# Performance work log

Hardware: AMD Instinct MI355X
Metric: run time of the kernel (lower is better)

## Reference

```python
import jax, jax.numpy as jnp
import numpy as np

EMBEDDING_DIM = 100
M = 50                      # chunk width
NUM_CHUNK = EMBEDDING_DIM // M  # 2
VOCAB = 100000
EPS = 1e-8                  # torch CosineSimilarity eps


def setup_inputs() -> dict:
    key = jax.random.key(0)
    k_idx, k_emb, k_w, k_u = jax.random.split(key, 4)
    word_idxs = jax.random.randint(k_idx, (4096, 200), 0, VOCAB)  # [B, L]
    # embedding table initialized uniform(-1, 1) as in the original np.random.uniform
    emb_table = jax.random.uniform(k_emb, (VOCAB, EMBEDDING_DIM), dtype=jnp.float32,
                                   minval=-1.0, maxval=1.0)
    weights = jnp.ones((EMBEDDING_DIM, 1), dtype=jnp.float32)      # output projection
    attend_u = jnp.ones((NUM_CHUNK, M), dtype=jnp.float32)         # per-chunk attention query
    return {"word_idxs": word_idxs, "emb_table": emb_table,
            "weights": weights, "attend_u": attend_u}


def reference(word_idxs, emb_table, weights, attend_u):
    B, L = word_idxs.shape
    embeds = emb_table[word_idxs]                       # [B, L, 100]
    ch = embeds.reshape(B, L, NUM_CHUNK, M)             # [B, L, C, M]
    # cosine similarity per word vs per-chunk query (torch eps semantics)
    e_norm = ch / jnp.maximum(jnp.linalg.norm(ch, axis=-1, keepdims=True), EPS)
    u_norm = attend_u / jnp.maximum(jnp.linalg.norm(attend_u, axis=-1, keepdims=True), EPS)
    cos = jnp.einsum('blcm,cm->blc', e_norm, u_norm)    # [B, L, C]
    alphas = jnp.exp(cos)                               # positive -> L1 norm == sum
    norm_alphas = alphas / jnp.sum(alphas, axis=1, keepdims=True)
    hidden = jnp.einsum('blcm,blc->bcm', ch, norm_alphas).reshape(B, EMBEDDING_DIM)
    return hidden @ weights                             # [B, 1]
```

## Files before the change

### kernel.cpp

```cpp
#include <hip/hip_runtime.h>

constexpr int C_ = 2;
constexpr int M_ = 50;
constexpr int ED = 100;
constexpr float EPS = 1e-8f;


__global__ __launch_bounds__(256) void row_stats_kernel(
    const float* __restrict__ emb,
    const float* __restrict__ wgt,
    const float* __restrict__ att,
    float*       __restrict__ tbl,
    int vocab)
{
    __shared__ float2 s_uw[ED];
    __shared__ float  s_su[C_];

    const int t = threadIdx.x;
    if (t < ED) s_uw[t] = make_float2(att[t], wgt[t]);
    __syncthreads();
    if (t < C_) {
        float ss = 0.f;
        #pragma unroll
        for (int m = 0; m < M_; ++m) { float v = s_uw[t * M_ + m].x; ss += v * v; }
        s_su[t] = 1.0f / fmaxf(sqrtf(ss), EPS);
    }
    __syncthreads();

    const int r = blockIdx.x * 256 + t;
    if (r >= vocab) return;

    const float4* rowp = reinterpret_cast<const float4*>(emb + (long long)r * ED);

    float sq0 = 0.f, du0 = 0.f, dw0 = 0.f;
    float sq1 = 0.f, du1 = 0.f, dw1 = 0.f;

    #pragma unroll
    for (int j = 0; j < 25; ++j) {
        const float4 v = rowp[j];
        const float vals[4] = { v.x, v.y, v.z, v.w };
        #pragma unroll
        for (int k = 0; k < 4; ++k) {
            const int e = 4 * j + k;
            const float2 uw = s_uw[e];
            const float x = vals[k];
            if (e < M_) {
                sq0 = fmaf(x, x, sq0);
                du0 = fmaf(x, uw.x, du0);
                dw0 = fmaf(x, uw.y, dw0);
            } else {
                sq1 = fmaf(x, x, sq1);
                du1 = fmaf(x, uw.x, du1);
                dw1 = fmaf(x, uw.y, dw1);
            }
        }
    }

    const float cos0 = du0 / fmaxf(sqrtf(sq0), EPS) * s_su[0];
    const float cos1 = du1 / fmaxf(sqrtf(sq1), EPS) * s_su[1];
    const float a0 = __expf(cos0);
    const float a1 = __expf(cos1);

    reinterpret_cast<float4*>(tbl)[r] = make_float4(a0, a0 * dw0, a1, a1 * dw1);
}

__global__ __launch_bounds__(256) void attend_kernel(
    const int*    __restrict__ idx,
    const float4* __restrict__ tbl,
    float*        __restrict__ out,
    int B, int L)
{
    const int wave = threadIdx.x >> 6;
    const int lane = threadIdx.x & 63;
    const int b    = blockIdx.x * 4 + wave;
    if (b >= B) return;

    const int* ib = idx + (long long)b * L;
    float a0 = 0.f, a1 = 0.f, ap0 = 0.f, ap1 = 0.f;
    #pragma unroll 4
    for (int l = lane; l < L; l += 64) {
        const float4 v = tbl[ib[l]];
        a0 += v.x; ap0 += v.y; a1 += v.z; ap1 += v.w;
    }

    #pragma unroll
    for (int off = 32; off > 0; off >>= 1) {
        a0  += __shfl_down(a0,  off, 64);
        a1  += __shfl_down(a1,  off, 64);
        ap0 += __shfl_down(ap0, off, 64);
        ap1 += __shfl_down(ap1, off, 64);
    }
    if (lane == 0) out[b] = ap0 / a0 + ap1 / a1;
}

extern "C" void kernel_launch(void* const* d_in, const int* in_sizes, int n_in,
                              void* d_out, int out_size, void* d_ws, size_t ws_size,
                              hipStream_t stream) {
    const int*   idx = (const int*)d_in[0];
    const float* emb = (const float*)d_in[1];
    const float* wgt = (const float*)d_in[2];
    const float* att = (const float*)d_in[3];
    float* out = (float*)d_out;

    const int B     = out_size;
    const int L     = in_sizes[0] / B;
    const int vocab = in_sizes[1] / ED;

    float* tbl = (float*)d_ws;

    row_stats_kernel<<<(vocab + 255) / 256, 256, 0, stream>>>(emb, wgt, att, tbl, vocab);
    attend_kernel<<<(B + 3) / 4, 256, 0, stream>>>(idx, (const float4*)tbl, out, B, L);
}
```

Baseline: 96.00 us.

## Split each embedding row across four lanes and use two waves per batch row

The row-stats kernel now gives each vocab row to four adjacent lanes. Each lane reads interleaved float4s and the partial sums are combined with xor shuffles, so global loads are more coalesced than the previous one-thread-per-row 400-byte strided reads. The attend kernel now spreads each batch row over two waves and combines them through shared memory, which gives more memory parallelism per row. In exchange it adds shuffle reductions, idle lanes during the tail and final writes, and a block-level sync.

Measured after the change: 92.54 us. 3.6% less time.

```diff
diff --git a/kernel.cpp b/kernel.cpp
--- a/kernel.cpp
+++ b/kernel.cpp
@@ -27,7 +27,11 @@
     }
     __syncthreads();
 
-    const int r = blockIdx.x * 256 + t;
+    const int wave = t >> 6;
+    const int lane = t & 63;
+    const int g    = lane >> 2;
+    const int j    = lane & 3;
+    const int r    = blockIdx.x * 64 + wave * 16 + g;
     if (r >= vocab) return;
 
     const float4* rowp = reinterpret_cast<const float4*>(emb + (long long)r * ED);
@@ -36,32 +40,51 @@
     float sq1 = 0.f, du1 = 0.f, dw1 = 0.f;
 
     #pragma unroll
-    for (int j = 0; j < 25; ++j) {
-        const float4 v = rowp[j];
-        const float vals[4] = { v.x, v.y, v.z, v.w };
+    for (int it = 0; it < 6; ++it) {
+        const float4 v = rowp[4 * it + j];
+        const float xs[4] = { v.x, v.y, v.z, v.w };
         #pragma unroll
         for (int k = 0; k < 4; ++k) {
-            const int e = 4 * j + k;
-            const float2 uw = s_uw[e];
-            const float x = vals[k];
-            if (e < M_) {
-                sq0 = fmaf(x, x, sq0);
-                du0 = fmaf(x, uw.x, du0);
-                dw0 = fmaf(x, uw.y, dw0);
+            const int ebase = 16 * it + k;
+            const float x   = xs[k];
+            const float2 uw = s_uw[ebase + 4 * j];
+            if (ebase + 12 < M_) {
+                sq0 = fmaf(x, x, sq0); du0 = fmaf(x, uw.x, du0); dw0 = fmaf(x, uw.y, dw0);
+            } else if (ebase >= M_) {
+                sq1 = fmaf(x, x, sq1); du1 = fmaf(x, uw.x, du1); dw1 = fmaf(x, uw.y, dw1);
             } else {
-                sq1 = fmaf(x, x, sq1);
-                du1 = fmaf(x, uw.x, du1);
-                dw1 = fmaf(x, uw.y, dw1);
+                if (j == 0) { sq0 = fmaf(x, x, sq0); du0 = fmaf(x, uw.x, du0); dw0 = fmaf(x, uw.y, dw0); }
+                else        { sq1 = fmaf(x, x, sq1); du1 = fmaf(x, uw.x, du1); dw1 = fmaf(x, uw.y, dw1); }
             }
         }
     }
+    if (j == 0) {
+        const float4 v = rowp[24];
+        const float xs[4] = { v.x, v.y, v.z, v.w };
+        #pragma unroll
+        for (int k = 0; k < 4; ++k) {
+            const float2 uw = s_uw[96 + k];
+            sq1 = fmaf(xs[k], xs[k], sq1); du1 = fmaf(xs[k], uw.x, du1); dw1 = fmaf(xs[k], uw.y, dw1);
+        }
+    }
 
-    const float cos0 = du0 / fmaxf(sqrtf(sq0), EPS) * s_su[0];
-    const float cos1 = du1 / fmaxf(sqrtf(sq1), EPS) * s_su[1];
-    const float a0 = __expf(cos0);
-    const float a1 = __expf(cos1);
+    #pragma unroll
+    for (int m = 1; m < 4; m <<= 1) {
+        sq0 += __shfl_xor(sq0, m, 4);
+        du0 += __shfl_xor(du0, m, 4);
+        dw0 += __shfl_xor(dw0, m, 4);
+        sq1 += __shfl_xor(sq1, m, 4);
+        du1 += __shfl_xor(du1, m, 4);
+        dw1 += __shfl_xor(dw1, m, 4);
+    }
 
-    reinterpret_cast<float4*>(tbl)[r] = make_float4(a0, a0 * dw0, a1, a1 * dw1);
+    if (j == 0) {
+        const float cos0 = du0 / fmaxf(sqrtf(sq0), EPS) * s_su[0];
+        const float cos1 = du1 / fmaxf(sqrtf(sq1), EPS) * s_su[1];
+        const float a0 = __expf(cos0);
+        const float a1 = __expf(cos1);
+        reinterpret_cast<float4*>(tbl)[r] = make_float4(a0, a0 * dw0, a1, a1 * dw1);
+    }
 }
 
 __global__ __launch_bounds__(256) void attend_kernel(
@@ -70,27 +93,38 @@
     float*        __restrict__ out,
     int B, int L)
 {
-    const int wave = threadIdx.x >> 6;
-    const int lane = threadIdx.x & 63;
-    const int b    = blockIdx.x * 4 + wave;
-    if (b >= B) return;
+    __shared__ float4 s_part[4];
 
-    const int* ib = idx + (long long)b * L;
-    float a0 = 0.f, a1 = 0.f, ap0 = 0.f, ap1 = 0.f;
-    #pragma unroll 4
-    for (int l = lane; l < L; l += 64) {
-        const float4 v = tbl[ib[l]];
-        a0 += v.x; ap0 += v.y; a1 += v.z; ap1 += v.w;
+    const int half = threadIdx.x >> 7;
+    const int tt   = threadIdx.x & 127;
+    const int b    = blockIdx.x * 2 + half;
+
+    float a0 = 0.f, ap0 = 0.f, a1 = 0.f, ap1 = 0.f;
+    if (b < B) {
+        const int* ib = idx + (long long)b * L;
+        #pragma unroll 2
+        for (int l = tt; l < L; l += 128) {
+            const float4 v = tbl[ib[l]];
+            a0 += v.x; ap0 += v.y; a1 += v.z; ap1 += v.w;
+        }
+        #pragma unroll
+        for (int off = 32; off > 0; off >>= 1) {
+            a0  += __shfl_down(a0,  off, 64);
+            a1  += __shfl_down(a1,  off, 64);
+            ap0 += __shfl_down(ap0, off, 64);
+            ap1 += __shfl_down(ap1, off, 64);
+        }
     }
 
-    #pragma unroll
-    for (int off = 32; off > 0; off >>= 1) {
-        a0  += __shfl_down(a0,  off, 64);
-        a1  += __shfl_down(a1,  off, 64);
-        ap0 += __shfl_down(ap0, off, 64);
-        ap1 += __shfl_down(ap1, off, 64);
+    const int wave = threadIdx.x >> 6;
+    if ((threadIdx.x & 63) == 0) s_part[wave] = make_float4(a0, ap0, a1, ap1);
+    __syncthreads();
+
+    if (tt == 0 && b < B) {
+        const float4 p = s_part[half * 2];
+        const float4 q = s_part[half * 2 + 1];
+        out[b] = (p.y + q.y) / (p.x + q.x) + (p.w + q.w) / (p.z + q.z);
     }
-    if (lane == 0) out[b] = ap0 / a0 + ap1 / a1;
 }
 
 extern "C" void kernel_launch(void* const* d_in, const int* in_sizes, int n_in,
@@ -108,6 +142,6 @@
 
     float* tbl = (float*)d_ws;
 
-    row_stats_kernel<<<(vocab + 255) / 256, 256, 0, stream>>>(emb, wgt, att, tbl, vocab);
-    attend_kernel<<<(B + 3) / 4, 256, 0, stream>>>(idx, (const float4*)tbl, out, B, L);
+    row_stats_kernel<<<(vocab + 63) / 64, 256, 0, stream>>>(emb, wgt, att, tbl, vocab);
+    attend_kernel<<<(B + 1) / 2, 256, 0, stream>>>(idx, (const float4*)tbl, out, B, L);
 }
```

## Split each vocab row across four lanes for coalesced row-stats loads

Applied to the files above, without the earlier changes.

The row-stats kernel now gives each vocab row to a group of four adjacent lanes, each handling two rows, instead of one whole row per thread. Neighbouring lanes read neighbouring float4s, so the 40MB embedding table is read with far better coalescing than the old strided per-thread 400-byte row walks. Partial sums are combined with 4-lane xor shuffles, and the chunk boundary that falls inside a float4 is handled by lane index. The cost is more shuffle work, extra registers, and some lane divergence on the tail float4.

New measurement: 93.06 us. 3.1% less time.

```diff
diff --git a/kernel.cpp b/kernel.cpp
--- a/kernel.cpp
+++ b/kernel.cpp
@@ -27,41 +27,97 @@
     }
     __syncthreads();
 
-    const int r = blockIdx.x * 256 + t;
-    if (r >= vocab) return;
+    const int wave = t >> 6;
+    const int lane = t & 63;
+    const int g    = lane >> 2;
+    const int j    = lane & 3;
+    const int rA   = blockIdx.x * 128 + wave * 32 + g;
+    const int rB   = rA + 16;
+    const bool okA = (rA < vocab);
+    const bool okB = (rB < vocab);
+    if (!okA) return;
 
-    const float4* rowp = reinterpret_cast<const float4*>(emb + (long long)r * ED);
+    const float4* rpA = reinterpret_cast<const float4*>(emb + (long long)rA * ED);
+    const float4* rpB = reinterpret_cast<const float4*>(emb + (long long)rB * ED);
 
-    float sq0 = 0.f, du0 = 0.f, dw0 = 0.f;
-    float sq1 = 0.f, du1 = 0.f, dw1 = 0.f;
+    float4 va[6], vb[6];
+    #pragma unroll
+    for (int it = 0; it < 6; ++it) va[it] = rpA[4 * it + j];
+    if (okB) {
+        #pragma unroll
+        for (int it = 0; it < 6; ++it) vb[it] = rpB[4 * it + j];
+    }
+    float4 ta, tb;
+    if (j == 0) {
+        ta = rpA[24];
+        if (okB) tb = rpB[24];
+    }
+
+    float AsQ0 = 0.f, AdU0 = 0.f, AdW0 = 0.f, AsQ1 = 0.f, AdU1 = 0.f, AdW1 = 0.f;
+    float BsQ0 = 0.f, BdU0 = 0.f, BdW0 = 0.f, BsQ1 = 0.f, BdU1 = 0.f, BdW1 = 0.f;
 
     #pragma unroll
-    for (int j = 0; j < 25; ++j) {
-        const float4 v = rowp[j];
-        const float vals[4] = { v.x, v.y, v.z, v.w };
+    for (int it = 0; it < 6; ++it) {
+        const float xsA[4] = { va[it].x, va[it].y, va[it].z, va[it].w };
+        const float xsB[4] = { vb[it].x, vb[it].y, vb[it].z, vb[it].w };
         #pragma unroll
         for (int k = 0; k < 4; ++k) {
-            const int e = 4 * j + k;
-            const float2 uw = s_uw[e];
-            const float x = vals[k];
-            if (e < M_) {
-                sq0 = fmaf(x, x, sq0);
-                du0 = fmaf(x, uw.x, du0);
-                dw0 = fmaf(x, uw.y, dw0);
+            const int ebase = 16 * it + k;
+            const float2 uw = s_uw[ebase + 4 * j];
+            const float xA = xsA[k];
+            const float xB = xsB[k];
+            if (ebase + 12 < M_) {
+                AsQ0 = fmaf(xA, xA, AsQ0); AdU0 = fmaf(xA, uw.x, AdU0); AdW0 = fmaf(xA, uw.y, AdW0);
+                BsQ0 = fmaf(xB, xB, BsQ0); BdU0 = fmaf(xB, uw.x, BdU0); BdW0 = fmaf(xB, uw.y, BdW0);
+            } else if (ebase >= M_) {
+                AsQ1 = fmaf(xA, xA, AsQ1); AdU1 = fmaf(xA, uw.x, AdU1); AdW1 = fmaf(xA, uw.y, AdW1);
+                BsQ1 = fmaf(xB, xB, BsQ1); BdU1 = fmaf(xB, uw.x, BdU1); BdW1 = fmaf(xB, uw.y, BdW1);
             } else {
-                sq1 = fmaf(x, x, sq1);
-                du1 = fmaf(x, uw.x, du1);
-                dw1 = fmaf(x, uw.y, dw1);
+                if (j == 0) {
+                    AsQ0 = fmaf(xA, xA, AsQ0); AdU0 = fmaf(xA, uw.x, AdU0); AdW0 = fmaf(xA, uw.y, AdW0);
+                    BsQ0 = fmaf(xB, xB, BsQ0); BdU0 = fmaf(xB, uw.x, BdU0); BdW0 = fmaf(xB, uw.y, BdW0);
+                } else {
+                    AsQ1 = fmaf(xA, xA, AsQ1); AdU1 = fmaf(xA, uw.x, AdU1); AdW1 = fmaf(xA, uw.y, AdW1);
+                    BsQ1 = fmaf(xB, xB, BsQ1); BdU1 = fmaf(xB, uw.x, BdU1); BdW1 = fmaf(xB, uw.y, BdW1);
+                }
             }
         }
     }
+    if (j == 0) {
+        const float xsA[4] = { ta.x, ta.y, ta.z, ta.w };
+        const float xsB[4] = { tb.x, tb.y, tb.z, tb.w };
+        #pragma unroll
+        for (int k = 0; k < 4; ++k) {
+            const float2 uw = s_uw[96 + k];
+            AsQ1 = fmaf(xsA[k], xsA[k], AsQ1); AdU1 = fmaf(xsA[k], uw.x, AdU1); AdW1 = fmaf(xsA[k], uw.y, AdW1);
+            BsQ1 = fmaf(xsB[k], xsB[k], BsQ1); BdU1 = fmaf(xsB[k], uw.x, BdU1); BdW1 = fmaf(xsB[k], uw.y, BdW1);
+        }
+    }
 
-    const float cos0 = du0 / fmaxf(sqrtf(sq0), EPS) * s_su[0];
-    const float cos1 = du1 / fmaxf(sqrtf(sq1), EPS) * s_su[1];
-    const float a0 = __expf(cos0);
-    const float a1 = __expf(cos1);
+    #pragma unroll
+    for (int m = 1; m < 4; m <<= 1) {
+        AsQ0 += __shfl_xor(AsQ0, m, 4); AdU0 += __shfl_xor(AdU0, m, 4); AdW0 += __shfl_xor(AdW0, m, 4);
+        AsQ1 += __shfl_xor(AsQ1, m, 4); AdU1 += __shfl_xor(AdU1, m, 4); AdW1 += __shfl_xor(AdW1, m, 4);
+        BsQ0 += __shfl_xor(BsQ0, m, 4); BdU0 += __shfl_xor(BdU0, m, 4); BdW0 += __shfl_xor(BdW0, m, 4);
+        BsQ1 += __shfl_xor(BsQ1, m, 4); BdU1 += __shfl_xor(BdU1, m, 4); BdW1 += __shfl_xor(BdW1, m, 4);
+    }
 
-    reinterpret_cast<float4*>(tbl)[r] = make_float4(a0, a0 * dw0, a1, a1 * dw1);
+    if (j == 0) {
+        {
+            const float cos0 = AdU0 / fmaxf(sqrtf(AsQ0), EPS) * s_su[0];
+            const float cos1 = AdU1 / fmaxf(sqrtf(AsQ1), EPS) * s_su[1];
+            const float a0 = __expf(cos0);
+            const float a1 = __expf(cos1);
+            reinterpret_cast<float4*>(tbl)[rA] = make_float4(a0, a0 * AdW0, a1, a1 * AdW1);
+        }
+        if (okB) {
+            const float cos0 = BdU0 / fmaxf(sqrtf(BsQ0), EPS) * s_su[0];
+            const float cos1 = BdU1 / fmaxf(sqrtf(BsQ1), EPS) * s_su[1];
+            const float a0 = __expf(cos0);
+            const float a1 = __expf(cos1);
+            reinterpret_cast<float4*>(tbl)[rB] = make_float4(a0, a0 * BdW0, a1, a1 * BdW1);
+        }
+    }
 }
 
 __global__ __launch_bounds__(256) void attend_kernel(
@@ -108,6 +164,6 @@
 
     float* tbl = (float*)d_ws;
 
-    row_stats_kernel<<<(vocab + 255) / 256, 256, 0, stream>>>(emb, wgt, att, tbl, vocab);
+    row_stats_kernel<<<(vocab + 127) / 128, 256, 0, stream>>>(emb, wgt, att, tbl, vocab);
     attend_kernel<<<(B + 3) / 4, 256, 0, stream>>>(idx, (const float4*)tbl, out, B, L);
 }
```

## Fuse row statistics and attention into one per-batch gather kernel

Applied to the files above, without the earlier changes.

Drops the per-vocabulary precomputation kernel and its workspace table. Each wave now handles one batch row: groups of four lanes gather a full 100-float embedding row, compute the chunk norms and dot products with shuffle reductions, and accumulate the exp-weighted sums directly. This removes a kernel launch and the pass over the whole table. In exchange it reads a full 400-byte row for every token instead of a 16-byte precomputed entry, and repeats the per-row maths for every occurrence of a word.

Measured after the change: 130.8 us. 1.36x slower.

```diff
diff --git a/kernel.cpp b/kernel.cpp
--- a/kernel.cpp
+++ b/kernel.cpp
@@ -5,92 +5,120 @@
 constexpr int ED = 100;
 constexpr float EPS = 1e-8f;
 
-
-__global__ __launch_bounds__(256) void row_stats_kernel(
+__global__ __launch_bounds__(256) void fused_direct_kernel(
+    const int*   __restrict__ idx,
     const float* __restrict__ emb,
     const float* __restrict__ wgt,
     const float* __restrict__ att,
-    float*       __restrict__ tbl,
-    int vocab)
+    float*       __restrict__ out,
+    int B, int L)
 {
-    __shared__ float2 s_uw[ED];
-    __shared__ float  s_su[C_];
+    __shared__ float s_su[C_];
 
     const int t = threadIdx.x;
-    if (t < ED) s_uw[t] = make_float2(att[t], wgt[t]);
-    __syncthreads();
     if (t < C_) {
         float ss = 0.f;
         #pragma unroll
-        for (int m = 0; m < M_; ++m) { float v = s_uw[t * M_ + m].x; ss += v * v; }
+        for (int m = 0; m < M_; ++m) { const float v = att[t * M_ + m]; ss += v * v; }
         s_su[t] = 1.0f / fmaxf(sqrtf(ss), EPS);
     }
     __syncthreads();
 
-    const int r = blockIdx.x * 256 + t;
-    if (r >= vocab) return;
+    const int wv   = t >> 6;
+    const int lane = t & 63;
+    const int g    = lane >> 2;
+    const int j    = lane & 3;
+    const int b    = blockIdx.x * 4 + wv;
+    if (b >= B) return;
 
-    const float4* rowp = reinterpret_cast<const float4*>(emb + (long long)r * ED);
+    const float su0 = s_su[0], su1 = s_su[1];
 
-    float sq0 = 0.f, du0 = 0.f, dw0 = 0.f;
-    float sq1 = 0.f, du1 = 0.f, dw1 = 0.f;
+    const float4* att4 = reinterpret_cast<const float4*>(att);
+    const float4* wgt4 = reinterpret_cast<const float4*>(wgt);
+    float4 uf[7], wf[7];
+    #pragma unroll
+    for (int k = 0; k < 7; ++k) {
+        const int f = j + 4 * k;
+        if (f < 25) { uf[k] = att4[f]; wf[k] = wgt4[f]; }
+        else        { uf[k] = make_float4(0.f,0.f,0.f,0.f); wf[k] = uf[k]; }
+    }
 
-    #pragma unroll
-    for (int j = 0; j < 25; ++j) {
-        const float4 v = rowp[j];
-        const float vals[4] = { v.x, v.y, v.z, v.w };
+    const int*    ib   = idx + (long long)b * L;
+    const float4* emb4 = reinterpret_cast<const float4*>(emb);
+
+    float A0 = 0.f, AP0 = 0.f, A1 = 0.f, AP1 = 0.f;
+
+    for (int base = 0; base < L; base += 256) {
+        int pre[4];
         #pragma unroll
-        for (int k = 0; k < 4; ++k) {
-            const int e = 4 * j + k;
-            const float2 uw = s_uw[e];
-            const float x = vals[k];
-            if (e < M_) {
-                sq0 = fmaf(x, x, sq0);
-                du0 = fmaf(x, uw.x, du0);
-                dw0 = fmaf(x, uw.y, dw0);
-            } else {
-                sq1 = fmaf(x, x, sq1);
-                du1 = fmaf(x, uw.x, du1);
-                dw1 = fmaf(x, uw.y, dw1);
+        for (int m = 0; m < 4; ++m) {
+            const int l0 = base + 64 * m + lane;
+            pre[m] = (l0 < L) ? ib[l0] : 0;
+        }
+        #pragma unroll
+        for (int i = 0; i < 16; ++i) {
+            if (base + 16 * i >= L) break;
+            const int ridx = __shfl(pre[i >> 2], 16 * (i & 3) + g, 64);
+            const int l    = base + 16 * i + g;
+            if (l < L) {
+                const float4* rp = emb4 + (long long)ridx * 25;
+                float4 rv[7];
+                #pragma unroll
+                for (int k = 0; k < 6; ++k) rv[k] = rp[j + 4 * k];
+                if (j == 0) rv[6] = rp[24];
+
+                float sq0 = 0.f, du0 = 0.f, dw0 = 0.f;
+                float sq1 = 0.f, du1 = 0.f, dw1 = 0.f;
+                #pragma unroll
+                for (int k = 0; k < 6; ++k) {
+                    const float xs[4] = { rv[k].x, rv[k].y, rv[k].z, rv[k].w };
+                    const float us[4] = { uf[k].x, uf[k].y, uf[k].z, uf[k].w };
+                    const float ws[4] = { wf[k].x, wf[k].y, wf[k].z, wf[k].w };
+                    #pragma unroll
+                    for (int c = 0; c < 4; ++c) {
+                        const float x = xs[c];
+                        if (k <= 2) {
+                            sq0 = fmaf(x, x, sq0); du0 = fmaf(x, us[c], du0); dw0 = fmaf(x, ws[c], dw0);
+                        } else if (k >= 4) {
+                            sq1 = fmaf(x, x, sq1); du1 = fmaf(x, us[c], du1); dw1 = fmaf(x, ws[c], dw1);
+                        } else {
+                            if (j == 0 && c < 2) { sq0 = fmaf(x, x, sq0); du0 = fmaf(x, us[c], du0); dw0 = fmaf(x, ws[c], dw0); }
+                            else                 { sq1 = fmaf(x, x, sq1); du1 = fmaf(x, us[c], du1); dw1 = fmaf(x, ws[c], dw1); }
+                        }
+                    }
+                }
+                if (j == 0) {
+                    const float xs[4] = { rv[6].x, rv[6].y, rv[6].z, rv[6].w };
+                    const float us[4] = { uf[6].x, uf[6].y, uf[6].z, uf[6].w };
+                    const float ws[4] = { wf[6].x, wf[6].y, wf[6].z, wf[6].w };
+                    #pragma unroll
+                    for (int c = 0; c < 4; ++c) {
+                        sq1 = fmaf(xs[c], xs[c], sq1); du1 = fmaf(xs[c], us[c], du1); dw1 = fmaf(xs[c], ws[c], dw1);
+                    }
+                }
+
+                #pragma unroll
+                for (int m = 1; m < 4; m <<= 1) {
+                    sq0 += __shfl_xor(sq0, m, 4); du0 += __shfl_xor(du0, m, 4); dw0 += __shfl_xor(dw0, m, 4);
+                    sq1 += __shfl_xor(sq1, m, 4); du1 += __shfl_xor(du1, m, 4); dw1 += __shfl_xor(dw1, m, 4);
+                }
+
+                const float a0 = __expf(du0 / fmaxf(sqrtf(sq0), EPS) * su0);
+                const float a1 = __expf(du1 / fmaxf(sqrtf(sq1), EPS) * su1);
+                A0 += a0; AP0 = fmaf(a0, dw0, AP0);
+                A1 += a1; AP1 = fmaf(a1, dw1, AP1);
             }
         }
     }
 
-    const float cos0 = du0 / fmaxf(sqrtf(sq0), EPS) * s_su[0];
-    const float cos1 = du1 / fmaxf(sqrtf(sq1), EPS) * s_su[1];
-    const float a0 = __expf(cos0);
-    const float a1 = __expf(cos1);
-
-    reinterpret_cast<float4*>(tbl)[r] = make_float4(a0, a0 * dw0, a1, a1 * dw1);
-}
-
-__global__ __launch_bounds__(256) void attend_kernel(
-    const int*    __restrict__ idx,
-    const float4* __restrict__ tbl,
-    float*        __restrict__ out,
-    int B, int L)
-{
-    const int wave = threadIdx.x >> 6;
-    const int lane = threadIdx.x & 63;
-    const int b    = blockIdx.x * 4 + wave;
-    if (b >= B) return;
-
-    const int* ib = idx + (long long)b * L;
-    float a0 = 0.f, a1 = 0.f, ap0 = 0.f, ap1 = 0.f;
-    #pragma unroll 4
-    for (int l = lane; l < L; l += 64) {
-        const float4 v = tbl[ib[l]];
-        a0 += v.x; ap0 += v.y; a1 += v.z; ap1 += v.w;
+    #pragma unroll
+    for (int off = 1; off < 64; off <<= 1) {
+        A0  += __shfl_xor(A0,  off, 64);
+        AP0 += __shfl_xor(AP0, off, 64);
+        A1  += __shfl_xor(A1,  off, 64);
+        AP1 += __shfl_xor(AP1, off, 64);
     }
-
-    #pragma unroll
-    for (int off = 32; off > 0; off >>= 1) {
-        a0  += __shfl_down(a0,  off, 64);
-        a1  += __shfl_down(a1,  off, 64);
-        ap0 += __shfl_down(ap0, off, 64);
-        ap1 += __shfl_down(ap1, off, 64);
-    }
-    if (lane == 0) out[b] = ap0 / a0 + ap1 / a1;
+    if (lane == 0) out[b] = AP0 / A0 + AP1 / A1;
 }
 
 extern "C" void kernel_launch(void* const* d_in, const int* in_sizes, int n_in,
@@ -102,12 +130,8 @@
     const float* att = (const float*)d_in[3];
     float* out = (float*)d_out;
 
-    const int B     = out_size;
-    const int L     = in_sizes[0] / B;
-    const int vocab = in_sizes[1] / ED;
+    const int B = out_size;
+    const int L = in_sizes[0] / B;
 
-    float* tbl = (float*)d_ws;
-
-    row_stats_kernel<<<(vocab + 255) / 256, 256, 0, stream>>>(emb, wgt, att, tbl, vocab);
-    attend_kernel<<<(B + 3) / 4, 256, 0, stream>>>(idx, (const float4*)tbl, out, B, L);
+    fused_direct_kernel<<<(B + 3) / 4, 256, 0, stream>>>(idx, emb, wgt, att, out, B, L);
 }
```
